# Kernel tuning notes

Measured on AMD Instinct MI355X. Metric: run time of the kernel, lower is better.

The kernel has to match this reference:

```python
import jax, jax.numpy as jnp
import numpy as np

D_MODEL = 1024
N_HEADS = 16
HEAD_DIM = D_MODEL // N_HEADS
WINDOW = 256


def setup_inputs() -> dict:
    key = jax.random.key(0)
    k1, k2, k3 = jax.random.split(key, 3)
    B, T = 4, 2048
    x = jax.random.normal(k1, (B, T, D_MODEL), dtype=jnp.float32)
    # weights stored as [in, out] (torch Linear does x @ W.T with W [out,in])
    scale_qkv = 1.0 / np.sqrt(D_MODEL)
    w_qkv = jax.random.normal(k2, (D_MODEL, 3 * D_MODEL), dtype=jnp.float32) * scale_qkv
    w_out = jax.random.normal(k3, (D_MODEL, D_MODEL), dtype=jnp.float32) * scale_qkv
    return {"x": x, "w_qkv": w_qkv, "w_out": w_out}


def _sliding_window_attention(x, w_qkv, w_out):
    B, T, C = x.shape
    qkv = x @ w_qkv                              # [B,T,3C]
    q, k, v = jnp.split(qkv, 3, axis=-1)

    def reshape(t):
        return t.reshape(B, T, N_HEADS, HEAD_DIM).transpose(0, 2, 1, 3)  # [B,H,T,Dh]

    q, k, v = reshape(q), reshape(k), reshape(v)

    # banded causal mask: position i attends to j in [i-WINDOW, i]
    pos = jnp.arange(T)
    dist = pos[None, :] - pos[:, None]           # dist[i,j] = j - i
    blocked = (dist > 0) | (dist < -WINDOW)      # True = blocked

    scale = 1.0 / np.sqrt(HEAD_DIM)
    scores = jnp.einsum('bhqd,bhkd->bhqk', q, k) * scale
    scores = jnp.where(blocked[None, None], -jnp.inf, scores)
    attn = jax.nn.softmax(scores, axis=-1)
    out = jnp.einsum('bhqk,bhkd->bhqd', attn, v)
    out = out.transpose(0, 2, 1, 3).reshape(B, T, C)
    return out @ w_out


def reference(x, w_qkv, w_out):
    return _sliding_window_attention(x, w_qkv, w_out)
```

## Files before the change

kernel.cpp:

```cpp
#include <hip/hip_runtime.h>
#include <stdint.h>

#define D_MODEL 1024
#define NHEADS  16
#define WINDOW  256
#define BATCH   4
#define SEQ     2048
#define NROWS   (BATCH*SEQ)

using short8 = __attribute__((ext_vector_type(8))) short;
using f32x4  = __attribute__((ext_vector_type(4))) float;
using u32x4  = __attribute__((ext_vector_type(4))) uint32_t;
using u16x4  = __attribute__((ext_vector_type(4))) unsigned short;
typedef unsigned short u16;

__device__ __forceinline__ u16 f2b(float f) {
  union { float f; uint32_t u; } v; v.f = f;
  uint32_t r = v.u + 0x7fffu + ((v.u >> 16) & 1u);
  return (u16)(r >> 16);
}

__device__ __forceinline__ void gload_lds16(const void* g, void* l) {
  __builtin_amdgcn_global_load_lds(
      (const __attribute__((address_space(1))) uint32_t*)g,
      (__attribute__((address_space(3))) uint32_t*)l, 16, 0, 0);
}

__device__ __forceinline__ void cvtT_body(const float* __restrict__ in, u16* __restrict__ out,
                                          int K, int C, int bn, int bk, int tid, float* T) {
#pragma unroll
  for (int it = 0; it < 4; ++it) {
    int c = it * 256 + tid;
    int k = c >> 4, g = c & 15;
    f32x4 v = *(const f32x4*)&in[(size_t)(bk * 64 + k) * C + bn * 64 + g * 4];
#pragma unroll
    for (int j = 0; j < 4; ++j) T[k * 65 + g * 4 + j] = v[j];
  }
  __syncthreads();
#pragma unroll
  for (int it = 0; it < 4; ++it) {
    int c = it * 256 + tid;
    int n = c >> 4, kg = c & 15;
    u16x4 o;
#pragma unroll
    for (int j = 0; j < 4; ++j) o[j] = f2b(T[(kg * 4 + j) * 65 + n]);
    *(u16x4*)&out[(size_t)(bn * 64 + n) * K + bk * 64 + kg * 4] = o;
  }
}

__global__ __launch_bounds__(256) void cvt_all_kernel(
    const float* __restrict__ x, const float* __restrict__ w_qkv, const float* __restrict__ w_out,
    u16* __restrict__ xb, u16* __restrict__ wqkvT, u16* __restrict__ woutT) {
  __shared__ float T[64 * 65];
  const int bid = blockIdx.x;
  const int tid = threadIdx.x;
  if (bid < 8192) {
    int i = bid * 256 + tid;
    f32x4 v = *(const f32x4*)(x + 4 * (size_t)i);
    u16x4 o;
    o.x = f2b(v.x); o.y = f2b(v.y); o.z = f2b(v.z); o.w = f2b(v.w);
    *(u16x4*)(xb + 4 * (size_t)i) = o;
  } else if (bid < 8192 + 768) {
    int b2 = bid - 8192;
    cvtT_body(w_qkv, wqkvT, D_MODEL, 3 * D_MODEL, b2 % 48, b2 / 48, tid, T);
  } else {
    int b3 = bid - 8960;
    cvtT_body(w_out, woutT, D_MODEL, D_MODEL, b3 % 16, b3 / 16, tid, T);
  }
}

template <int MODE>
__global__ __launch_bounds__(512, 2) void gemm256_kernel(
    const u16* __restrict__ A, const u16* __restrict__ BT,
    u16* __restrict__ qk, u16* __restrict__ vT, float* __restrict__ outf,
    int M, int N, int K, int nbx) {
  __shared__ short SM[3 * 24576];

  const int tid = threadIdx.x;
  const int l = tid & 63;
  const int w = tid >> 6;
  const int wm = w >> 1, wn = w & 1;
  const int lr = l & 15, q = l >> 4;
  const int gsw = lr & 7;

  const int nwg = gridDim.x;
  const int lid = blockIdx.x;
  const int wg = (lid & 7) * (nwg >> 3) + (lid >> 3);
  const int bx = wg % nbx, by = wg / nbx;
  const int m0 = by * 256, n0 = bx * 128;

  const int NT = K >> 6;

  f32x4 acc[4][4] = {};

  auto stageA = [&](int slot, int kt) {
    short* As = SM + slot * 24576;
#pragma unroll
    for (int i = 0; i < 4; ++i) {
      int c = i * 512 + tid;
      int row = c >> 3;
      int gs = (c & 7) ^ (row & 7);
      gload_lds16(A + (size_t)(m0 + row) * K + (kt << 6) + gs * 8,
                  &As[(i * 512 + w * 64) * 8]);
    }
  };
  auto stageB = [&](int slot, int kt) {
    short* Bs = SM + slot * 24576 + 16384;
#pragma unroll
    for (int i = 0; i < 2; ++i) {
      int c = i * 512 + tid;
      int row = c >> 3;
      int gs = (c & 7) ^ (row & 7);
      gload_lds16(BT + (size_t)(n0 + row) * K + (kt << 6) + gs * 8,
                  &Bs[(i * 512 + w * 64) * 8]);
    }
  };

  stageA(0, 0); stageB(0, 0);
  stageA(1, 1); stageB(1, 1);

  int slot = 0;
  for (int t = 0; t < NT; ++t) {
    if (t + 1 < NT) { asm volatile("s_waitcnt vmcnt(6)" ::: "memory"); }
    else            { asm volatile("s_waitcnt vmcnt(0)" ::: "memory"); }
    __builtin_amdgcn_s_barrier();

    const short* As = SM + slot * 24576;
    const short* Bs = As + 16384;
    int s2 = slot + 2; if (s2 >= 3) s2 -= 3;
    const bool st = (t + 2 < NT);

#pragma unroll
    for (int kh = 0; kh < 2; ++kh) {
      short8 af[4], bfr[4];
      const int ko = (((kh << 2) | q) ^ gsw) * 8;
#pragma unroll
      for (int mf = 0; mf < 4; ++mf)
        af[mf] = *(const short8*)&As[(wm * 64 + mf * 16 + lr) * 64 + ko];
#pragma unroll
      for (int nf = 0; nf < 4; ++nf)
        bfr[nf] = *(const short8*)&Bs[(wn * 64 + nf * 16 + lr) * 64 + ko];
      if (st) { if (kh == 0) stageA(s2, t + 2); else stageB(s2, t + 2); }
      __builtin_amdgcn_s_barrier();
      asm volatile("s_waitcnt lgkmcnt(0)" ::: "memory");
      __builtin_amdgcn_s_setprio(1);
#pragma unroll
      for (int mf = 0; mf < 4; ++mf)
#pragma unroll
        for (int nf = 0; nf < 4; ++nf)
          acc[mf][nf] = __builtin_amdgcn_mfma_f32_16x16x32_bf16(af[mf], bfr[nf], acc[mf][nf], 0, 0, 0);
      __builtin_amdgcn_s_setprio(0);
    }
    slot = (slot + 1 == 3) ? 0 : slot + 1;
  }

  if (MODE == 1) {
#pragma unroll
    for (int mf = 0; mf < 4; ++mf) {
      const int m = m0 + wm * 64 + mf * 16 + q * 4;
#pragma unroll
      for (int nf = 0; nf < 4; ++nf) {
        const int n = n0 + wn * 64 + nf * 16 + lr;
#pragma unroll
        for (int r = 0; r < 4; ++r)
          outf[(size_t)(m + r) * N + n] = acc[mf][nf][r];
      }
    }
    return;
  }

  if (n0 < 2048) {
#pragma unroll
    for (int mf = 0; mf < 4; ++mf) {
      const int m = m0 + wm * 64 + mf * 16 + q * 4;
#pragma unroll
      for (int nf = 0; nf < 4; ++nf) {
        const int n = n0 + wn * 64 + nf * 16 + lr;
#pragma unroll
        for (int r = 0; r < 4; ++r)
          qk[(size_t)(m + r) * 2048 + n] = f2b(acc[mf][nf][r]);
      }
    }
  } else {
    __syncthreads();
    short* Tw = SM + w * 1152;
    const int b = by >> 3;
    const int head = (n0 - 2048 + wn * 64) >> 6;
    const int t0 = (by & 7) * 256 + wm * 64;
    const size_t dbase = ((size_t)(b * NHEADS + head)) * 64;
#pragma unroll
    for (int nf = 0; nf < 4; ++nf) {
#pragma unroll
      for (int mf = 0; mf < 4; ++mf)
#pragma unroll
        for (int r = 0; r < 4; ++r)
          Tw[lr * 72 + mf * 16 + q * 4 + r] = (short)f2b(acc[mf][nf][r]);
      asm volatile("s_waitcnt lgkmcnt(0)" ::: "memory");
#pragma unroll
      for (int it = 0; it < 2; ++it) {
        int c = it * 64 + l;
        int row = c >> 3, off = (c & 7) * 8;
        short8 v = *(const short8*)&Tw[row * 72 + off];
        *(short8*)&vT[(dbase + nf * 16 + row) * 2048 + t0 + off] = v;
      }
      asm volatile("s_waitcnt lgkmcnt(0)" ::: "memory");
    }
  }
}

__global__ __launch_bounds__(512) void attn_kernel(
    const u16* __restrict__ qk, const u16* __restrict__ vT, u16* __restrict__ attn) {
  __shared__ short Ks[2][64 * 72];
  __shared__ short Vs[2][64 * 72];
  __shared__ short Ps[8 * 16 * 72];

  const int tid = threadIdx.x;
  const int l = tid & 63;
  const int w = tid >> 6;
  const int wset = w >> 2;
  const int wl = w & 3;

  const int lid = blockIdx.x;
  const int xcd = lid & 7, slot = lid >> 3;
  const int bh = (slot >> 4) * 8 + xcd;
  const int qt2 = slot & 15;
  const int qtA = qt2 * 2;
  const int myqt = qtA + wset;
  const int qbase = myqt * 64;
  const int b = bh >> 4, h = bh & 15;
  const size_t rowbase = (size_t)b * 2048;
  const int lr = l & 15, lk = (l >> 4) * 8;

  const int srow = tid >> 3, soff = (tid & 7) * 8;

  u32x4 kreg, vreg;
  auto load_regs = [&](int kt) {
    const int kbase = kt * 64;
    kreg = *(const u32x4*)&qk[(rowbase + kbase + srow) * 2048 + 1024 + h * 64 + soff];
    vreg = *(const u32x4*)&vT[((size_t)bh * 64 + srow) * 2048 + kbase + soff];
  };
  auto write_lds = [&](int buf) {
    *(u32x4*)&Ks[buf][srow * 72 + soff] = kreg;
    *(u32x4*)&Vs[buf][srow * 72 + soff] = vreg;
  };

  const size_t qrowg = (rowbase + qbase + wl * 16 + lr) * 2048 + h * 64;
  short8 aq0 = *(const short8*)&qk[qrowg + lk];
  short8 aq1 = *(const short8*)&qk[qrowg + 32 + lk];

  float lsum[4] = {0.f, 0.f, 0.f, 0.f};
  f32x4 o[4] = {};

  int ktlo = qtA - 4; if (ktlo < 0) ktlo = 0;
  const int kthi = qtA + 1;

  load_regs(ktlo);
  write_lds(0);
  load_regs(ktlo + 1);
  asm volatile("s_waitcnt lgkmcnt(0)" ::: "memory");
  __builtin_amdgcn_s_barrier();

  short* Pw = &Ps[w * 16 * 72];
  int cur = 0;
  for (int kt = ktlo; kt <= kthi; ++kt) {
    const int kbase = kt * 64;
    const bool active = wset ? (kt >= myqt - 4) : (kt <= myqt);

    if (active) {
      f32x4 s[4] = {};
      __builtin_amdgcn_s_setprio(1);
#pragma unroll
      for (int fn = 0; fn < 4; ++fn) {
        short8 bk0 = *(const short8*)&Ks[cur][(fn * 16 + lr) * 72 + lk];
        short8 bk1 = *(const short8*)&Ks[cur][(fn * 16 + lr) * 72 + 32 + lk];
        s[fn] = __builtin_amdgcn_mfma_f32_16x16x32_bf16(aq0, bk0, s[fn], 0, 0, 0);
        s[fn] = __builtin_amdgcn_mfma_f32_16x16x32_bf16(aq1, bk1, s[fn], 0, 0, 0);
      }
      __builtin_amdgcn_s_setprio(0);

      f32x4 p[4];
      if (kt == myqt || kt == myqt - 4) {
        const int qrow0 = qbase + wl * 16 + (l >> 4) * 4;
#pragma unroll
        for (int fn = 0; fn < 4; ++fn) {
          int kj = kbase + fn * 16 + lr;
#pragma unroll
          for (int r = 0; r < 4; ++r) {
            int qi = qrow0 + r;
            bool ok = (kj <= qi) && (kj >= qi - WINDOW);
            p[fn][r] = ok ? __expf(s[fn][r] * 0.125f) : 0.f;
          }
        }
      } else {
#pragma unroll
        for (int fn = 0; fn < 4; ++fn)
#pragma unroll
          for (int r = 0; r < 4; ++r)
            p[fn][r] = __expf(s[fn][r] * 0.125f);
      }
#pragma unroll
      for (int r = 0; r < 4; ++r)
        lsum[r] += (p[0][r] + p[1][r]) + (p[2][r] + p[3][r]);

#pragma unroll
      for (int fn = 0; fn < 4; ++fn)
#pragma unroll
        for (int r = 0; r < 4; ++r)
          Pw[((l >> 4) * 4 + r) * 72 + fn * 16 + lr] = (short)f2b(p[fn][r]);
      asm volatile("s_waitcnt lgkmcnt(0)" ::: "memory");

      __builtin_amdgcn_s_setprio(1);
#pragma unroll
      for (int ks = 0; ks < 2; ++ks) {
        short8 pa = *(const short8*)&Pw[lr * 72 + ks * 32 + lk];
#pragma unroll
        for (int fd = 0; fd < 4; ++fd) {
          short8 vb = *(const short8*)&Vs[cur][(fd * 16 + lr) * 72 + ks * 32 + lk];
          o[fd] = __builtin_amdgcn_mfma_f32_16x16x32_bf16(pa, vb, o[fd], 0, 0, 0);
        }
      }
      __builtin_amdgcn_s_setprio(0);
      asm volatile("s_waitcnt lgkmcnt(0)" ::: "memory");
    }

    if (kt + 1 <= kthi) {
      write_lds(cur ^ 1);
      if (kt + 2 <= kthi) load_regs(kt + 2);
      asm volatile("s_waitcnt lgkmcnt(0)" ::: "memory");
      __builtin_amdgcn_s_barrier();
      cur ^= 1;
    }
  }

#pragma unroll
  for (int off = 1; off < 16; off <<= 1)
#pragma unroll
    for (int r = 0; r < 4; ++r) lsum[r] += __shfl_xor(lsum[r], off);

#pragma unroll
  for (int fd = 0; fd < 4; ++fd) {
#pragma unroll
    for (int r = 0; r < 4; ++r) {
      int m = qbase + wl * 16 + (l >> 4) * 4 + r;
      float val = o[fd][r] / lsum[r];
      attn[(rowbase + m) * 1024 + h * 64 + fd * 16 + lr] = f2b(val);
    }
  }
}

extern "C" void kernel_launch(void* const* d_in, const int* in_sizes, int n_in,
                              void* d_out, int out_size, void* d_ws, size_t ws_size,
                              hipStream_t stream) {
  const float* x     = (const float*)d_in[0];
  const float* w_qkv = (const float*)d_in[1];
  const float* w_out = (const float*)d_in[2];
  float* out = (float*)d_out;
  uint8_t* ws = (uint8_t*)d_ws;

  u16* xb    = (u16*)(ws + 0);
  u16* wqkvT = (u16*)(ws + 16777216);
  u16* woutT = (u16*)(ws + 23068672);
  u16* qk    = (u16*)(ws + 25165824);
  u16* vT    = (u16*)(ws + 58720256);

  cvt_all_kernel<<<8192 + 768 + 256, 256, 0, stream>>>(x, w_qkv, w_out, xb, wqkvT, woutT);

  gemm256_kernel<0><<<(3 * D_MODEL / 128) * (NROWS / 256), 512, 0, stream>>>(
      xb, wqkvT, qk, vT, nullptr, NROWS, 3 * D_MODEL, D_MODEL, 3 * D_MODEL / 128);

  attn_kernel<<<BATCH * NHEADS * (SEQ / 128), 512, 0, stream>>>(qk, vT, xb);

  gemm256_kernel<1><<<(D_MODEL / 128) * (NROWS / 256), 512, 0, stream>>>(
      xb, woutT, nullptr, nullptr, out, NROWS, D_MODEL, D_MODEL, D_MODEL / 128);
}
```

Measured before the change: 123.7 us.

## Fuse fp32-to-bf16 conversion of x into the QKV GEMM A-tile load

The separate pass that converts x to bf16 is removed. The QKV GEMM now loads fp32 A tiles into registers, converts them to bf16, and writes them to double-buffered LDS, while B keeps its async global-to-LDS pipeline. This saves writing and re-reading a 16MB bf16 copy of x and one kernel's worth of bandwidth. In exchange, each A tile is read twice in fp32 (24 column blocks instead of once), register pressure goes up, and the A loads are now synchronous register loads instead of direct-to-LDS loads.

```diff
diff --git a/kernel.cpp b/kernel.cpp
--- a/kernel.cpp
+++ b/kernel.cpp
@@ -48,33 +48,25 @@
   }
 }
 
-__global__ __launch_bounds__(256) void cvt_all_kernel(
-    const float* __restrict__ x, const float* __restrict__ w_qkv, const float* __restrict__ w_out,
-    u16* __restrict__ xb, u16* __restrict__ wqkvT, u16* __restrict__ woutT) {
+__global__ __launch_bounds__(256) void cvt_w_kernel(
+    const float* __restrict__ w_qkv, const float* __restrict__ w_out,
+    u16* __restrict__ wqkvT, u16* __restrict__ woutT) {
   __shared__ float T[64 * 65];
   const int bid = blockIdx.x;
   const int tid = threadIdx.x;
-  if (bid < 8192) {
-    int i = bid * 256 + tid;
-    f32x4 v = *(const f32x4*)(x + 4 * (size_t)i);
-    u16x4 o;
-    o.x = f2b(v.x); o.y = f2b(v.y); o.z = f2b(v.z); o.w = f2b(v.w);
-    *(u16x4*)(xb + 4 * (size_t)i) = o;
-  } else if (bid < 8192 + 768) {
-    int b2 = bid - 8192;
-    cvtT_body(w_qkv, wqkvT, D_MODEL, 3 * D_MODEL, b2 % 48, b2 / 48, tid, T);
+  if (bid < 768) {
+    cvtT_body(w_qkv, wqkvT, D_MODEL, 3 * D_MODEL, bid % 48, bid / 48, tid, T);
   } else {
-    int b3 = bid - 8960;
+    int b3 = bid - 768;
     cvtT_body(w_out, woutT, D_MODEL, D_MODEL, b3 % 16, b3 / 16, tid, T);
   }
 }
 
-template <int MODE>
-__global__ __launch_bounds__(512, 2) void gemm256_kernel(
-    const u16* __restrict__ A, const u16* __restrict__ BT,
-    u16* __restrict__ qk, u16* __restrict__ vT, float* __restrict__ outf,
-    int M, int N, int K, int nbx) {
-  __shared__ short SM[3 * 24576];
+__global__ __launch_bounds__(512, 2) void gemm_qkv_kernel(
+    const float* __restrict__ Af, const u16* __restrict__ BT,
+    u16* __restrict__ qk, u16* __restrict__ vT) {
+  __shared__ short SA[2 * 16384];
+  __shared__ short SB[3 * 8192];
 
   const int tid = threadIdx.x;
   const int l = tid & 63;
@@ -86,6 +78,148 @@
   const int nwg = gridDim.x;
   const int lid = blockIdx.x;
   const int wg = (lid & 7) * (nwg >> 3) + (lid >> 3);
+  const int bx = wg % 24, by = wg / 24;
+  const int m0 = by * 256, n0 = bx * 128;
+
+  const int NT = 16;
+
+  f32x4 acc[4][4] = {};
+  f32x4 ar[4][2];
+
+  auto loadAregs = [&](int kt) {
+    const int kk = kt << 6;
+#pragma unroll
+    for (int i = 0; i < 4; ++i) {
+      int c = i * 512 + tid;
+      int row = c >> 3;
+      int gs = (c & 7) ^ (row & 7);
+      const float* src = Af + (size_t)(m0 + row) * 1024 + kk + gs * 8;
+      ar[i][0] = *(const f32x4*)src;
+      ar[i][1] = *(const f32x4*)(src + 4);
+    }
+  };
+  auto writeA = [&](int aslot) {
+    short* As = SA + aslot * 16384;
+#pragma unroll
+    for (int i = 0; i < 4; ++i) {
+      int c = i * 512 + tid;
+      short8 v;
+#pragma unroll
+      for (int j = 0; j < 4; ++j) {
+        v[j]     = (short)f2b(ar[i][0][j]);
+        v[4 + j] = (short)f2b(ar[i][1][j]);
+      }
+      *(short8*)&As[c * 8] = v;
+    }
+  };
+  auto stageB = [&](int slot, int kt) {
+    short* Bs = SB + slot * 8192;
+#pragma unroll
+    for (int i = 0; i < 2; ++i) {
+      int c = i * 512 + tid;
+      int row = c >> 3;
+      int gs = (c & 7) ^ (row & 7);
+      gload_lds16(BT + (size_t)(n0 + row) * 1024 + (kt << 6) + gs * 8,
+                  &Bs[(i * 512 + w * 64) * 8]);
+    }
+  };
+
+  loadAregs(0);
+  stageB(0, 0);
+  stageB(1, 1);
+
+  int aslot = 0, bslot = 0;
+  for (int t = 0; t < NT; ++t) {
+    if (t == NT - 1) { asm volatile("s_waitcnt vmcnt(0)" ::: "memory"); }
+    else             { asm volatile("s_waitcnt vmcnt(2)" ::: "memory"); }
+    writeA(aslot);
+    asm volatile("s_waitcnt lgkmcnt(0)" ::: "memory");
+    __builtin_amdgcn_s_barrier();
+
+    const short* As = SA + aslot * 16384;
+    const short* Bs = SB + bslot * 8192;
+    int bs2 = bslot + 2; if (bs2 >= 3) bs2 -= 3;
+
+#pragma unroll
+    for (int kh = 0; kh < 2; ++kh) {
+      short8 af[4], bfr[4];
+      const int ko = (((kh << 2) | q) ^ gsw) * 8;
+#pragma unroll
+      for (int mf = 0; mf < 4; ++mf)
+        af[mf] = *(const short8*)&As[(wm * 64 + mf * 16 + lr) * 64 + ko];
+#pragma unroll
+      for (int nf = 0; nf < 4; ++nf)
+        bfr[nf] = *(const short8*)&Bs[(wn * 64 + nf * 16 + lr) * 64 + ko];
+      if (kh == 0) { if (t + 1 < NT) loadAregs(t + 1); }
+      else         { if (t + 2 < NT) stageB(bs2, t + 2); }
+      __builtin_amdgcn_s_barrier();
+      asm volatile("s_waitcnt lgkmcnt(0)" ::: "memory");
+      __builtin_amdgcn_s_setprio(1);
+#pragma unroll
+      for (int mf = 0; mf < 4; ++mf)
+#pragma unroll
+        for (int nf = 0; nf < 4; ++nf)
+          acc[mf][nf] = __builtin_amdgcn_mfma_f32_16x16x32_bf16(af[mf], bfr[nf], acc[mf][nf], 0, 0, 0);
+      __builtin_amdgcn_s_setprio(0);
+    }
+    aslot ^= 1;
+    bslot = (bslot + 1 == 3) ? 0 : bslot + 1;
+  }
+
+  if (n0 < 2048) {
+#pragma unroll
+    for (int mf = 0; mf < 4; ++mf) {
+      const int m = m0 + wm * 64 + mf * 16 + q * 4;
+#pragma unroll
+      for (int nf = 0; nf < 4; ++nf) {
+        const int n = n0 + wn * 64 + nf * 16 + lr;
+#pragma unroll
+        for (int r = 0; r < 4; ++r)
+          qk[(size_t)(m + r) * 2048 + n] = f2b(acc[mf][nf][r]);
+      }
+    }
+  } else {
+    __syncthreads();
+    short* Tw = SA + w * 1152;
+    const int b = by >> 3;
+    const int head = (n0 - 2048 + wn * 64) >> 6;
+    const int t0 = (by & 7) * 256 + wm * 64;
+    const size_t dbase = ((size_t)(b * NHEADS + head)) * 64;
+#pragma unroll
+    for (int nf = 0; nf < 4; ++nf) {
+#pragma unroll
+      for (int mf = 0; mf < 4; ++mf)
+#pragma unroll
+        for (int r = 0; r < 4; ++r)
+          Tw[lr * 72 + mf * 16 + q * 4 + r] = (short)f2b(acc[mf][nf][r]);
+      asm volatile("s_waitcnt lgkmcnt(0)" ::: "memory");
+#pragma unroll
+      for (int it = 0; it < 2; ++it) {
+        int c = it * 64 + l;
+        int row = c >> 3, off = (c & 7) * 8;
+        short8 v = *(const short8*)&Tw[row * 72 + off];
+        *(short8*)&vT[(dbase + nf * 16 + row) * 2048 + t0 + off] = v;
+      }
+      asm volatile("s_waitcnt lgkmcnt(0)" ::: "memory");
+    }
+  }
+}
+
+__global__ __launch_bounds__(512, 2) void gemm_out_kernel(
+    const u16* __restrict__ A, const u16* __restrict__ BT, float* __restrict__ outf,
+    int M, int N, int K, int nbx) {
+  __shared__ short SM[3 * 24576];
+
+  const int tid = threadIdx.x;
+  const int l = tid & 63;
+  const int w = tid >> 6;
+  const int wm = w >> 1, wn = w & 1;
+  const int lr = l & 15, q = l >> 4;
+  const int gsw = lr & 7;
+
+  const int nwg = gridDim.x;
+  const int lid = blockIdx.x;
+  const int wg = (lid & 7) * (nwg >> 3) + (lid >> 3);
   const int bx = wg % nbx, by = wg / nbx;
   const int m0 = by * 256, n0 = bx * 128;
 
@@ -154,56 +288,15 @@
     slot = (slot + 1 == 3) ? 0 : slot + 1;
   }
 
-  if (MODE == 1) {
-#pragma unroll
-    for (int mf = 0; mf < 4; ++mf) {
-      const int m = m0 + wm * 64 + mf * 16 + q * 4;
-#pragma unroll
-      for (int nf = 0; nf < 4; ++nf) {
-        const int n = n0 + wn * 64 + nf * 16 + lr;
-#pragma unroll
-        for (int r = 0; r < 4; ++r)
-          outf[(size_t)(m + r) * N + n] = acc[mf][nf][r];
-      }
-    }
-    return;
-  }
-
-  if (n0 < 2048) {
-#pragma unroll
-    for (int mf = 0; mf < 4; ++mf) {
-      const int m = m0 + wm * 64 + mf * 16 + q * 4;
-#pragma unroll
-      for (int nf = 0; nf < 4; ++nf) {
-        const int n = n0 + wn * 64 + nf * 16 + lr;
-#pragma unroll
-        for (int r = 0; r < 4; ++r)
-          qk[(size_t)(m + r) * 2048 + n] = f2b(acc[mf][nf][r]);
-      }
-    }
-  } else {
-    __syncthreads();
-    short* Tw = SM + w * 1152;
-    const int b = by >> 3;
-    const int head = (n0 - 2048 + wn * 64) >> 6;
-    const int t0 = (by & 7) * 256 + wm * 64;
-    const size_t dbase = ((size_t)(b * NHEADS + head)) * 64;
+#pragma unroll
+  for (int mf = 0; mf < 4; ++mf) {
+    const int m = m0 + wm * 64 + mf * 16 + q * 4;
 #pragma unroll
     for (int nf = 0; nf < 4; ++nf) {
-#pragma unroll
-      for (int mf = 0; mf < 4; ++mf)
-#pragma unroll
-        for (int r = 0; r < 4; ++r)
-          Tw[lr * 72 + mf * 16 + q * 4 + r] = (short)f2b(acc[mf][nf][r]);
-      asm volatile("s_waitcnt lgkmcnt(0)" ::: "memory");
-#pragma unroll
-      for (int it = 0; it < 2; ++it) {
-        int c = it * 64 + l;
-        int row = c >> 3, off = (c & 7) * 8;
-        short8 v = *(const short8*)&Tw[row * 72 + off];
-        *(short8*)&vT[(dbase + nf * 16 + row) * 2048 + t0 + off] = v;
-      }
-      asm volatile("s_waitcnt lgkmcnt(0)" ::: "memory");
+      const int n = n0 + wn * 64 + nf * 16 + lr;
+#pragma unroll
+      for (int r = 0; r < 4; ++r)
+        outf[(size_t)(m + r) * N + n] = acc[mf][nf][r];
     }
   }
 }
@@ -357,19 +450,18 @@
   float* out = (float*)d_out;
   uint8_t* ws = (uint8_t*)d_ws;
 
-  u16* xb    = (u16*)(ws + 0);
+  u16* attnb = (u16*)(ws + 0);
   u16* wqkvT = (u16*)(ws + 16777216);
   u16* woutT = (u16*)(ws + 23068672);
   u16* qk    = (u16*)(ws + 25165824);
   u16* vT    = (u16*)(ws + 58720256);
 
-  cvt_all_kernel<<<8192 + 768 + 256, 256, 0, stream>>>(x, w_qkv, w_out, xb, wqkvT, woutT);
-
-  gemm256_kernel<0><<<(3 * D_MODEL / 128) * (NROWS / 256), 512, 0, stream>>>(
-      xb, wqkvT, qk, vT, nullptr, NROWS, 3 * D_MODEL, D_MODEL, 3 * D_MODEL / 128);
-
-  attn_kernel<<<BATCH * NHEADS * (SEQ / 128), 512, 0, stream>>>(qk, vT, xb);
-
-  gemm256_kernel<1><<<(D_MODEL / 128) * (NROWS / 256), 512, 0, stream>>>(
-      xb, woutT, nullptr, nullptr, out, NROWS, D_MODEL, D_MODEL, D_MODEL / 128);
-}
+  cvt_w_kernel<<<1024, 256, 0, stream>>>(w_qkv, w_out, wqkvT, woutT);
+
+  gemm_qkv_kernel<<<768, 512, 0, stream>>>(x, wqkvT, qk, vT);
+
+  attn_kernel<<<BATCH * NHEADS * (SEQ / 128), 512, 0, stream>>>(qk, vT, attnb);
+
+  gemm_out_kernel<<<(D_MODEL / 128) * (NROWS / 256), 512, 0, stream>>>(
+      attnb, woutT, out, NROWS, D_MODEL, D_MODEL, D_MODEL / 128);
+}
```

Measured after the change: 142.4 us. 15.1% more time.
